# Performance work log

Hardware: AMD Instinct MI355X
Metric: run time of the kernel (lower is better)

The kernel has to match this reference:

```python
import jax, jax.numpy as jnp
import numpy as np

N_NODES = 100000
N_EDGES = 500000
H = 128
EPS = 1e-5


def _mlp(x, W1, b1, W2, b2, W3, b3, g, beta):
    # 3-layer MLP (ReLU) + final LayerNorm, matching build_mlp(..., lay_norm=True, n_layers=3)
    h = jax.nn.relu(x @ W1 + b1)
    h = jax.nn.relu(h @ W2 + b2)
    h = h @ W3 + b3
    mu = jnp.mean(h, axis=-1, keepdims=True)
    var = jnp.var(h, axis=-1, keepdims=True)
    return (h - mu) * jax.lax.rsqrt(var + EPS) * g + beta


def setup_inputs() -> dict:
    key = jax.random.key(0)
    ks = jax.random.split(key, 20)
    s = lambda fan_in: 1.0 / np.sqrt(fan_in)
    inp = {
        "x": jax.random.normal(ks[0], (N_NODES, H), dtype=jnp.float32),
        "edge_attr": jax.random.normal(ks[1], (N_EDGES, H), dtype=jnp.float32),
        "edge_index": jax.random.randint(ks[2], (2, N_EDGES), 0, N_NODES, dtype=jnp.int64),
        # Edge MLP: in = 3H
        "eW1": jax.random.normal(ks[3], (3 * H, H), dtype=jnp.float32) * s(3 * H),
        "eb1": jnp.zeros((H,), jnp.float32),
        "eW2": jax.random.normal(ks[4], (H, H), dtype=jnp.float32) * s(H),
        "eb2": jnp.zeros((H,), jnp.float32),
        "eW3": jax.random.normal(ks[5], (H, H), dtype=jnp.float32) * s(H),
        "eb3": jnp.zeros((H,), jnp.float32),
        "eg": jnp.ones((H,), jnp.float32),
        "ebeta": jnp.zeros((H,), jnp.float32),
        # Node MLP: in = 2H
        "nW1": jax.random.normal(ks[6], (2 * H, H), dtype=jnp.float32) * s(2 * H),
        "nb1": jnp.zeros((H,), jnp.float32),
        "nW2": jax.random.normal(ks[7], (H, H), dtype=jnp.float32) * s(H),
        "nb2": jnp.zeros((H,), jnp.float32),
        "nW3": jax.random.normal(ks[8], (H, H), dtype=jnp.float32) * s(H),
        "nb3": jnp.zeros((H,), jnp.float32),
        "ng": jnp.ones((H,), jnp.float32),
        "nbeta": jnp.zeros((H,), jnp.float32),
    }
    return inp


def reference(x, edge_attr, edge_index,
              eW1, eb1, eW2, eb2, eW3, eb3, eg, ebeta,
              nW1, nb1, nW2, nb2, nW3, nb3, ng, nbeta):
    senders = edge_index[0]
    receivers = edge_index[1]
    # EdgeBlock: gather src/dst node feats, concat with edge feats, MLP (3H -> H)
    e_in = jnp.concatenate([x[senders], x[receivers], edge_attr], axis=-1)
    e_new = _mlp(e_in, eW1, eb1, eW2, eb2, eW3, eb3, eg, ebeta)
    # NodeBlock: scatter-sum edge messages to receiver nodes, concat with node feats, MLP (2H -> H)
    agg = jax.ops.segment_sum(e_new, receivers, num_segments=N_NODES)
    n_in = jnp.concatenate([x, agg], axis=-1)
    x_new = _mlp(n_in, nW1, nb1, nW2, nb2, nW3, nb3, ng, nbeta)
    # Residual connections
    return (x + x_new, edge_attr + e_new)
```

## Files before the change

### kernel.cpp

```cpp
#include <hip/hip_runtime.h>

#define N_NODES 100000
#define N_EDGES 500000
#define H 128
#define EPS 1e-5f

typedef __attribute__((ext_vector_type(8))) short bf16x8;
typedef __attribute__((ext_vector_type(4))) float f32x4;

__device__ __forceinline__ unsigned short f2bf(float f) {
  unsigned int u = __builtin_bit_cast(unsigned int, f);
  u += 0x7FFFu + ((u >> 16) & 1u);
  return (unsigned short)(u >> 16);
}
__device__ __forceinline__ float bf2f(unsigned short u) {
  return __builtin_bit_cast(float, (unsigned)u << 16);
}

__device__ __forceinline__ int swz(int r, int k) {
  return r * 128 + (k ^ ((r & 7) << 3));
}

union PK8 { unsigned short u[8]; uint4 q; };

#define GLDS16(g, l)                                                        \
  __builtin_amdgcn_global_load_lds(                                         \
      (const __attribute__((address_space(1))) void*)(g),                   \
      (__attribute__((address_space(3))) void*)(l), 16, 0, 0)

__device__ __forceinline__ void stage_w512(unsigned short* dst,
                                           const unsigned short* img) {
  const int t = threadIdx.x;
  #pragma unroll
  for (int j = 0; j < 4; ++j)
    GLDS16((const char*)img + j * 8192 + t * 16, (char*)dst + j * 8192 + t * 16);
}

__device__ __forceinline__ void gemm_regA(const bf16x8 a[4], const unsigned short* Wb,
                                          int m0, int kq, f32x4 acc[8]) {
  #pragma unroll
  for (int kk = 0; kk < 4; ++kk) {
    const int k0 = kk * 32 + kq * 8;
    #pragma unroll
    for (int tc = 0; tc < 8; ++tc) {
      bf16x8 b = *(const bf16x8*)&Wb[swz(tc * 16 + m0, k0)];
      acc[tc] = __builtin_amdgcn_mfma_f32_16x16x32_bf16(a[kk], b, acc[tc], 0, 0, 0);
    }
  }
}

__device__ __forceinline__ void gemm_ldsA(const unsigned short* Hb, int wrow,
                                          const unsigned short* Wb,
                                          int m0, int kq, f32x4 acc[8]) {
  #pragma unroll
  for (int kk = 0; kk < 4; ++kk) {
    const int k0 = kk * 32 + kq * 8;
    bf16x8 a = *(const bf16x8*)&Hb[swz(wrow + m0, k0)];
    #pragma unroll
    for (int tc = 0; tc < 8; ++tc) {
      bf16x8 b = *(const bf16x8*)&Wb[swz(tc * 16 + m0, k0)];
      acc[tc] = __builtin_amdgcn_mfma_f32_16x16x32_bf16(a, b, acc[tc], 0, 0, 0);
    }
  }
}

__device__ __forceinline__ void zero_acc(f32x4 acc[8]) {
  #pragma unroll
  for (int b = 0; b < 8; ++b) acc[b] = (f32x4){0.f, 0.f, 0.f, 0.f};
}

__device__ __forceinline__ void write_h(unsigned short* Hb, const f32x4 acc[8],
                                        const float* __restrict__ bias,
                                        int wrow, int m0, int kq) {
  #pragma unroll
  for (int tc = 0; tc < 8; ++tc) {
    const int col = tc * 16 + m0;
    const float b = bias[col];
    #pragma unroll
    for (int i = 0; i < 4; ++i)
      Hb[swz(wrow + kq * 4 + i, col)] = f2bf(fmaxf(acc[tc][i] + b, 0.0f));
  }
}

__device__ __forceinline__ void ln4(const f32x4 acc[8], float mu[4], float rv[4]) {
  float s[4] = {0, 0, 0, 0}, ss[4] = {0, 0, 0, 0};
  #pragma unroll
  for (int tc = 0; tc < 8; ++tc)
    #pragma unroll
    for (int i = 0; i < 4; ++i) {
      const float v = acc[tc][i];
      s[i] += v;
      ss[i] += v * v;
    }
  #pragma unroll
  for (int off = 1; off < 16; off <<= 1)
    #pragma unroll
    for (int i = 0; i < 4; ++i) {
      s[i] += __shfl_xor(s[i], off);
      ss[i] += __shfl_xor(ss[i], off);
    }
  #pragma unroll
  for (int i = 0; i < 4; ++i) {
    const float m = s[i] * (1.0f / 128.0f);
    const float var = ss[i] * (1.0f / 128.0f) - m * m;
    mu[i] = m;
    rv[i] = rsqrtf(var + EPS);
  }
}


__global__ void xprep_kernel(const float* __restrict__ x,
                             unsigned short* __restrict__ xb) {
  const long i = (long)blockIdx.x * 256 + threadIdx.x;
  const long base = i * 8;
  if (base < (long)N_NODES * H) {
    float4 v0 = *(const float4*)(x + base);
    float4 v1 = *(const float4*)(x + base + 4);
    PK8 pk;
    pk.u[0] = f2bf(v0.x); pk.u[1] = f2bf(v0.y);
    pk.u[2] = f2bf(v0.z); pk.u[3] = f2bf(v0.w);
    pk.u[4] = f2bf(v1.x); pk.u[5] = f2bf(v1.y);
    pk.u[6] = f2bf(v1.z); pk.u[7] = f2bf(v1.w);
    *(uint4*)(xb + base) = pk.q;
  }
}

struct WSrc { const float* p[9]; };

__global__ void wprep_kernel(WSrc wsrc, unsigned short* __restrict__ wimg) {
  const int id = blockIdx.x * 256 + threadIdx.x;
  const int m = id >> 14;
  const int r = id & 16383;
  const int n = r & 127;
  const int k = r >> 7;
  wimg[m * 16384 + swz(n, k)] = f2bf(wsrc.p[m][k * 128 + n]);
}


__global__ void hist_kernel(const int* __restrict__ ridx, unsigned* __restrict__ cnt) {
  const int e = blockIdx.x * 256 + threadIdx.x;
  if (e < N_EDGES) atomicAdd(&cnt[ridx[e]], 1u);
}

__global__ void scan1_kernel(const unsigned* __restrict__ cnt,
                             unsigned* __restrict__ offs,
                             unsigned* __restrict__ part) {
  __shared__ unsigned sh[256];
  const int t = threadIdx.x;
  const int base = blockIdx.x * 1024 + t * 4;
  unsigned v[4];
  #pragma unroll
  for (int i = 0; i < 4; ++i) v[i] = (base + i < N_NODES) ? cnt[base + i] : 0u;
  unsigned pre[4];
  pre[0] = 0; pre[1] = v[0]; pre[2] = v[0] + v[1]; pre[3] = pre[2] + v[2];
  const unsigned tot = pre[3] + v[3];
  sh[t] = tot;
  __syncthreads();
  for (int d = 1; d < 256; d <<= 1) {
    const unsigned u_ = (t >= d) ? sh[t - d] : 0u;
    __syncthreads();
    sh[t] += u_;
    __syncthreads();
  }
  const unsigned excl = sh[t] - tot;
  #pragma unroll
  for (int i = 0; i < 4; ++i)
    if (base + i < N_NODES) offs[base + i] = excl + pre[i];
  if (t == 255) part[blockIdx.x] = sh[255];
}

__global__ void scan2_kernel(unsigned* __restrict__ part, int n) {
  __shared__ unsigned sh[128];
  const int t = threadIdx.x;
  const unsigned v = (t < n) ? part[t] : 0u;
  sh[t] = v;
  __syncthreads();
  for (int d = 1; d < 128; d <<= 1) {
    const unsigned u_ = (t >= d) ? sh[t - d] : 0u;
    __syncthreads();
    sh[t] += u_;
    __syncthreads();
  }
  if (t < n) part[t] = sh[t] - v;
}

__global__ void scan3_kernel(unsigned* __restrict__ offs,
                             const unsigned* __restrict__ part,
                             unsigned* __restrict__ cursor) {
  const int i = blockIdx.x * 256 + threadIdx.x;
  if (i < N_NODES) {
    const unsigned o = offs[i] + part[i >> 10];
    offs[i] = o;
    cursor[i] = o;
  }
  if (i == 0) offs[N_NODES] = N_EDGES;
}

__global__ void scatter_kernel(const int* __restrict__ ridx,
                               unsigned* __restrict__ cursor,
                               unsigned* __restrict__ eord) {
  const int e = blockIdx.x * 256 + threadIdx.x;
  if (e < N_EDGES) {
    const unsigned p = atomicAdd(&cursor[ridx[e]], 1u);
    eord[p] = (unsigned)e;
  }
}


__global__ __launch_bounds__(512, 4) void edge_kernel(
    const unsigned short* __restrict__ xb, const float* __restrict__ edge_attr,
    const int* __restrict__ eidx, const unsigned short* __restrict__ wimg,
    const float* __restrict__ eb1, const float* __restrict__ eb2,
    const float* __restrict__ eb3,
    const float* __restrict__ eg, const float* __restrict__ ebeta,
    float* __restrict__ out_e, unsigned short* __restrict__ enew) {
  __shared__ unsigned short Wbuf[128 * 128];
  __shared__ unsigned short Hbuf[128 * 128];

  const int t = threadIdx.x;
  const int lane = t & 63;
  const int wave = t >> 6;
  const int wrow = wave * 16;
  const int m0 = lane & 15;
  const int kq = lane >> 4;
  const long e0 = (long)blockIdx.x * 128;
  const int* sidx = eidx;
  const int* ridx = eidx + N_EDGES;

  stage_w512(Wbuf, wimg + 0L * 16384);
  stage_w512(Hbuf, wimg + 1L * 16384);

  long erow = e0 + wrow + m0;
  if (erow > N_EDGES - 1) erow = N_EDGES - 1;
  const long ns = sidx[erow];
  const long nr = ridx[erow];
  bf16x8 aS[4], aR[4];
  {
    const unsigned short* ps = xb + ns * H + kq * 8;
    const unsigned short* pr = xb + nr * H + kq * 8;
    #pragma unroll
    for (int kk = 0; kk < 4; ++kk) {
      aS[kk] = *(const bf16x8*)(ps + kk * 32);
      aR[kk] = *(const bf16x8*)(pr + kk * 32);
    }
  }

  f32x4 acc[8];
  zero_acc(acc);

  __syncthreads();
  gemm_regA(aS, Wbuf, m0, kq, acc);
  gemm_regA(aR, Hbuf, m0, kq, acc);

  bf16x8 aE[4];
  {
    const float* pe = edge_attr + erow * (long)H + kq * 8;
    #pragma unroll
    for (int kk = 0; kk < 4; ++kk) {
      float4 v0 = *(const float4*)(pe + kk * 32);
      float4 v1 = *(const float4*)(pe + kk * 32 + 4);
      PK8 pk;
      pk.u[0] = f2bf(v0.x); pk.u[1] = f2bf(v0.y);
      pk.u[2] = f2bf(v0.z); pk.u[3] = f2bf(v0.w);
      pk.u[4] = f2bf(v1.x); pk.u[5] = f2bf(v1.y);
      pk.u[6] = f2bf(v1.z); pk.u[7] = f2bf(v1.w);
      aE[kk] = __builtin_bit_cast(bf16x8, pk.q);
    }
  }

  __syncthreads();
  stage_w512(Wbuf, wimg + 2L * 16384);
  __syncthreads();
  gemm_regA(aE, Wbuf, m0, kq, acc);

  __syncthreads();
  stage_w512(Wbuf, wimg + 3L * 16384);
  write_h(Hbuf, acc, eb1, wrow, m0, kq);
  zero_acc(acc);
  __syncthreads();
  gemm_ldsA(Hbuf, wrow, Wbuf, m0, kq, acc);

  __syncthreads();
  stage_w512(Wbuf, wimg + 4L * 16384);
  write_h(Hbuf, acc, eb2, wrow, m0, kq);
  zero_acc(acc);
  __syncthreads();
  gemm_ldsA(Hbuf, wrow, Wbuf, m0, kq, acc);

  float gm[8], bt[8];
  #pragma unroll
  for (int tc = 0; tc < 8; ++tc) {
    const int col = tc * 16 + m0;
    const float b3 = eb3[col];
    gm[tc] = eg[col];
    bt[tc] = ebeta[col];
    #pragma unroll
    for (int i = 0; i < 4; ++i) acc[tc][i] += b3;
  }
  float mu[4], rv[4];
  ln4(acc, mu, rv);

  __syncthreads();
  #pragma unroll
  for (int tc = 0; tc < 8; ++tc) {
    const int col = tc * 16 + m0;
    #pragma unroll
    for (int i = 0; i < 4; ++i) {
      const float y = (acc[tc][i] - mu[i]) * rv[i] * gm[tc] + bt[tc];
      Hbuf[swz(wrow + kq * 4 + i, col)] = f2bf(y);
    }
  }
  __syncthreads();

  {
    const int r = t >> 2;
    const int c0 = (t & 3) * 32;
    const long e = e0 + r;
    if (e < N_EDGES) {
      const float* ea = edge_attr + e * (long)H + c0;
      float* oe = out_e + e * (long)H + c0;
      unsigned short* en = enew + e * (long)H + c0;
      #pragma unroll
      for (int c2 = 0; c2 < 4; ++c2) {
        uint4 qv = *(const uint4*)&Hbuf[swz(r, c0 + c2 * 8)];
        *(uint4*)(en + c2 * 8) = qv;
        const unsigned short* pu = (const unsigned short*)&qv;
        float4 a0 = *(const float4*)(ea + c2 * 8);
        float4 a1 = *(const float4*)(ea + c2 * 8 + 4);
        float4 o0, o1;
        o0.x = a0.x + bf2f(pu[0]); o0.y = a0.y + bf2f(pu[1]);
        o0.z = a0.z + bf2f(pu[2]); o0.w = a0.w + bf2f(pu[3]);
        o1.x = a1.x + bf2f(pu[4]); o1.y = a1.y + bf2f(pu[5]);
        o1.z = a1.z + bf2f(pu[6]); o1.w = a1.w + bf2f(pu[7]);
        *(float4*)(oe + c2 * 8) = o0;
        *(float4*)(oe + c2 * 8 + 4) = o1;
      }
    }
  }
}

__global__ __launch_bounds__(512, 4) void node_kernel(
    const unsigned short* __restrict__ xb, const float* __restrict__ x,
    const unsigned short* __restrict__ enew,
    const unsigned* __restrict__ offs, const unsigned* __restrict__ eord,
    const unsigned short* __restrict__ wimg,
    const float* __restrict__ nb1, const float* __restrict__ nb2,
    const float* __restrict__ nb3,
    const float* __restrict__ ng, const float* __restrict__ nbeta,
    float* __restrict__ out_x) {
  __shared__ unsigned short Wbuf[128 * 128];
  __shared__ unsigned short Hbuf[128 * 128];

  const int t = threadIdx.x;
  const int lane = t & 63;
  const int wave = t >> 6;
  const int wrow = wave * 16;
  const int m0 = lane & 15;
  const int kq = lane >> 4;
  const long n0 = (long)blockIdx.x * 128;

  stage_w512(Wbuf, wimg + 5L * 16384);

  long nrow = n0 + wrow + m0;
  if (nrow > N_NODES - 1) nrow = N_NODES - 1;
  bf16x8 aX[4];
  {
    const unsigned short* px = xb + nrow * H + kq * 8;
    #pragma unroll
    for (int kk = 0; kk < 4; ++kk) aX[kk] = *(const bf16x8*)(px + kk * 32);
  }

  float av[32];
  #pragma unroll
  for (int i = 0; i < 32; ++i) av[i] = 0.f;
  {
    const long sn = n0 + (t >> 2);
    if (sn < N_NODES) {
      const unsigned o0 = offs[sn], o1 = offs[sn + 1];
      const int c0 = (t & 3) * 32;
      for (unsigned u_ = o0; u_ < o1; ++u_) {
        const unsigned short* er = enew + (long)eord[u_] * H + c0;
        #pragma unroll
        for (int c2 = 0; c2 < 4; ++c2) {
          uint4 qv = *(const uint4*)(er + c2 * 8);
          const unsigned short* pu = (const unsigned short*)&qv;
          #pragma unroll
          for (int j = 0; j < 8; ++j) av[c2 * 8 + j] += bf2f(pu[j]);
        }
      }
    }
  }

  f32x4 acc[8];
  zero_acc(acc);

  __syncthreads();
  gemm_regA(aX, Wbuf, m0, kq, acc);
  __syncthreads();
  stage_w512(Wbuf, wimg + 6L * 16384);
  {
    const int r = t >> 2;
    const int c0 = (t & 3) * 32;
    #pragma unroll
    for (int c2 = 0; c2 < 4; ++c2) {
      PK8 pk;
      #pragma unroll
      for (int j = 0; j < 8; ++j) pk.u[j] = f2bf(av[c2 * 8 + j]);
      *(uint4*)&Hbuf[swz(r, c0 + c2 * 8)] = pk.q;
    }
  }
  __syncthreads();
  gemm_ldsA(Hbuf, wrow, Wbuf, m0, kq, acc);

  __syncthreads();
  stage_w512(Wbuf, wimg + 7L * 16384);
  write_h(Hbuf, acc, nb1, wrow, m0, kq);
  zero_acc(acc);
  __syncthreads();
  gemm_ldsA(Hbuf, wrow, Wbuf, m0, kq, acc);

  __syncthreads();
  stage_w512(Wbuf, wimg + 8L * 16384);
  write_h(Hbuf, acc, nb2, wrow, m0, kq);
  zero_acc(acc);
  __syncthreads();
  gemm_ldsA(Hbuf, wrow, Wbuf, m0, kq, acc);

  float gm[8], bt[8];
  #pragma unroll
  for (int tc = 0; tc < 8; ++tc) {
    const int col = tc * 16 + m0;
    const float b3 = nb3[col];
    gm[tc] = ng[col];
    bt[tc] = nbeta[col];
    #pragma unroll
    for (int i = 0; i < 4; ++i) acc[tc][i] += b3;
  }
  float mu[4], rv[4];
  ln4(acc, mu, rv);

  __syncthreads();
  #pragma unroll
  for (int tc = 0; tc < 8; ++tc) {
    const int col = tc * 16 + m0;
    #pragma unroll
    for (int i = 0; i < 4; ++i) {
      const float y = (acc[tc][i] - mu[i]) * rv[i] * gm[tc] + bt[tc];
      Hbuf[swz(wrow + kq * 4 + i, col)] = f2bf(y);
    }
  }
  __syncthreads();

  {
    const int r = t >> 2;
    const int c0 = (t & 3) * 32;
    const long n = n0 + r;
    if (n < N_NODES) {
      const float* xr = x + n * (long)H + c0;
      float* ox = out_x + n * (long)H + c0;
      #pragma unroll
      for (int c2 = 0; c2 < 4; ++c2) {
        uint4 qv = *(const uint4*)&Hbuf[swz(r, c0 + c2 * 8)];
        const unsigned short* pu = (const unsigned short*)&qv;
        float4 a0 = *(const float4*)(xr + c2 * 8);
        float4 a1 = *(const float4*)(xr + c2 * 8 + 4);
        float4 o0, o1;
        o0.x = a0.x + bf2f(pu[0]); o0.y = a0.y + bf2f(pu[1]);
        o0.z = a0.z + bf2f(pu[2]); o0.w = a0.w + bf2f(pu[3]);
        o1.x = a1.x + bf2f(pu[4]); o1.y = a1.y + bf2f(pu[5]);
        o1.z = a1.z + bf2f(pu[6]); o1.w = a1.w + bf2f(pu[7]);
        *(float4*)(ox + c2 * 8) = o0;
        *(float4*)(ox + c2 * 8 + 4) = o1;
      }
    }
  }
}

extern "C" void kernel_launch(void* const* d_in, const int* in_sizes, int n_in,
                              void* d_out, int out_size, void* d_ws, size_t ws_size,
                              hipStream_t stream) {
  (void)in_sizes; (void)n_in; (void)out_size; (void)ws_size;
  const float* x         = (const float*)d_in[0];
  const float* edge_attr = (const float*)d_in[1];
  const int*   eidx      = (const int*)d_in[2];
  const float* eW1 = (const float*)d_in[3];
  const float* eb1 = (const float*)d_in[4];
  const float* eW2 = (const float*)d_in[5];
  const float* eb2 = (const float*)d_in[6];
  const float* eW3 = (const float*)d_in[7];
  const float* eb3 = (const float*)d_in[8];
  const float* eg  = (const float*)d_in[9];
  const float* ebt = (const float*)d_in[10];
  const float* nW1 = (const float*)d_in[11];
  const float* nb1 = (const float*)d_in[12];
  const float* nW2 = (const float*)d_in[13];
  const float* nb2 = (const float*)d_in[14];
  const float* nW3 = (const float*)d_in[15];
  const float* nb3 = (const float*)d_in[16];
  const float* ng  = (const float*)d_in[17];
  const float* nbt = (const float*)d_in[18];

  float* out_x = (float*)d_out;
  float* out_e = (float*)d_out + (size_t)N_NODES * H;

  char* w = (char*)d_ws;
  unsigned short* enew = (unsigned short*)(w + 0);
  unsigned short* xb   = (unsigned short*)(w + 128000000);
  unsigned short* wimg = (unsigned short*)(w + 153600000);
  unsigned* offs   = (unsigned*)(w + 153894912);
  unsigned* cnt    = (unsigned*)(w + 154295040);
  unsigned* cursor = (unsigned*)(w + 154695168);
  unsigned* part   = (unsigned*)(w + 155095296);
  unsigned* eord   = (unsigned*)(w + 155096320);

  const int* ridx = eidx + N_EDGES;

  hipMemsetAsync(cnt, 0, (size_t)N_NODES * sizeof(unsigned), stream);

  WSrc wsrc;
  wsrc.p[0] = eW1;
  wsrc.p[1] = eW1 + 16384;
  wsrc.p[2] = eW1 + 32768;
  wsrc.p[3] = eW2;
  wsrc.p[4] = eW3;
  wsrc.p[5] = nW1;
  wsrc.p[6] = nW1 + 16384;
  wsrc.p[7] = nW2;
  wsrc.p[8] = nW3;

  xprep_kernel<<<(N_NODES * H / 8 + 255) / 256, 256, 0, stream>>>(x, xb);
  wprep_kernel<<<576, 256, 0, stream>>>(wsrc, wimg);

  hist_kernel<<<(N_EDGES + 255) / 256, 256, 0, stream>>>(ridx, cnt);
  scan1_kernel<<<(N_NODES + 1023) / 1024, 256, 0, stream>>>(cnt, offs, part);
  scan2_kernel<<<1, 128, 0, stream>>>(part, (N_NODES + 1023) / 1024);
  scan3_kernel<<<(N_NODES + 255) / 256, 256, 0, stream>>>(offs, part, cursor);
  scatter_kernel<<<(N_EDGES + 255) / 256, 256, 0, stream>>>(ridx, cursor, eord);

  const int eblocks = (N_EDGES + 127) / 128;
  const int nblocks = (N_NODES + 127) / 128;
  edge_kernel<<<eblocks, 512, 0, stream>>>(xb, edge_attr, eidx, wimg, eb1, eb2, eb3,
                                           eg, ebt, out_e, enew);
  node_kernel<<<nblocks, 512, 0, stream>>>(xb, x, enew, offs, eord, wimg,
                                           nb1, nb2, nb3, ng, nbt, out_x);
}
```

Before: 459.0 us.

## Precompute per-node first-layer projections and use persistent CSR-sorted edge/node kernels

```diff
diff --git a/kernel.cpp b/kernel.cpp
--- a/kernel.cpp
+++ b/kernel.cpp
@@ -4,6 +4,9 @@
 #define N_EDGES 500000
 #define H 128
 #define EPS 1e-5f
+#define NT_E 1954
+#define NT_N 391
+#define PGRID 256
 
 typedef __attribute__((ext_vector_type(8))) short bf16x8;
 typedef __attribute__((ext_vector_type(4))) float f32x4;
@@ -28,14 +31,6 @@
       (const __attribute__((address_space(1))) void*)(g),                   \
       (__attribute__((address_space(3))) void*)(l), 16, 0, 0)
 
-__device__ __forceinline__ void stage_w512(unsigned short* dst,
-                                           const unsigned short* img) {
-  const int t = threadIdx.x;
-  #pragma unroll
-  for (int j = 0; j < 4; ++j)
-    GLDS16((const char*)img + j * 8192 + t * 16, (char*)dst + j * 8192 + t * 16);
-}
-
 __device__ __forceinline__ void gemm_regA(const bf16x8 a[4], const unsigned short* Wb,
                                           int m0, int kq, f32x4 acc[8]) {
   #pragma unroll
@@ -67,19 +62,6 @@
 __device__ __forceinline__ void zero_acc(f32x4 acc[8]) {
   #pragma unroll
   for (int b = 0; b < 8; ++b) acc[b] = (f32x4){0.f, 0.f, 0.f, 0.f};
-}
-
-__device__ __forceinline__ void write_h(unsigned short* Hb, const f32x4 acc[8],
-                                        const float* __restrict__ bias,
-                                        int wrow, int m0, int kq) {
-  #pragma unroll
-  for (int tc = 0; tc < 8; ++tc) {
-    const int col = tc * 16 + m0;
-    const float b = bias[col];
-    #pragma unroll
-    for (int i = 0; i < 4; ++i)
-      Hb[swz(wrow + kq * 4 + i, col)] = f2bf(fmaxf(acc[tc][i] + b, 0.0f));
-  }
 }
 
 __device__ __forceinline__ void ln4(const f32x4 acc[8], float mu[4], float rv[4]) {
@@ -108,22 +90,6 @@
   }
 }
 
-
-__global__ void xprep_kernel(const float* __restrict__ x,
-                             unsigned short* __restrict__ xb) {
-  const long i = (long)blockIdx.x * 256 + threadIdx.x;
-  const long base = i * 8;
-  if (base < (long)N_NODES * H) {
-    float4 v0 = *(const float4*)(x + base);
-    float4 v1 = *(const float4*)(x + base + 4);
-    PK8 pk;
-    pk.u[0] = f2bf(v0.x); pk.u[1] = f2bf(v0.y);
-    pk.u[2] = f2bf(v0.z); pk.u[3] = f2bf(v0.w);
-    pk.u[4] = f2bf(v1.x); pk.u[5] = f2bf(v1.y);
-    pk.u[6] = f2bf(v1.z); pk.u[7] = f2bf(v1.w);
-    *(uint4*)(xb + base) = pk.q;
-  }
-}
 
 struct WSrc { const float* p[9]; };
 
@@ -134,6 +100,86 @@
   const int n = r & 127;
   const int k = r >> 7;
   wimg[m * 16384 + swz(n, k)] = f2bf(wsrc.p[m][k * 128 + n]);
+}
+
+
+__global__ __launch_bounds__(512, 2) void px_kernel(
+    const float* __restrict__ x, const unsigned short* __restrict__ wimg,
+    const float* __restrict__ eb1, const float* __restrict__ nb1,
+    unsigned short* __restrict__ pxs, unsigned short* __restrict__ pxr,
+    unsigned short* __restrict__ pxn) {
+  extern __shared__ unsigned short smem[];
+  const int t = threadIdx.x;
+  #pragma unroll
+  for (int j = 0; j < 12; ++j)
+    GLDS16((const char*)wimg + j * 8192 + t * 16, (char*)smem + j * 8192 + t * 16);
+  __syncthreads();
+
+  const int lane = t & 63;
+  const int wtile = (t >> 6) * 16;
+  const int m0 = lane & 15;
+  const int kq = lane >> 4;
+  const long n0 = (long)blockIdx.x * 128;
+
+  long an = n0 + wtile + m0;
+  if (an > N_NODES - 1) an = N_NODES - 1;
+  const float* px_ = x + an * H + kq * 8;
+  bf16x8 aX[4];
+  #pragma unroll
+  for (int kk = 0; kk < 4; ++kk) {
+    float4 v0 = *(const float4*)(px_ + kk * 32);
+    float4 v1 = *(const float4*)(px_ + kk * 32 + 4);
+    PK8 pk;
+    pk.u[0] = f2bf(v0.x); pk.u[1] = f2bf(v0.y);
+    pk.u[2] = f2bf(v0.z); pk.u[3] = f2bf(v0.w);
+    pk.u[4] = f2bf(v1.x); pk.u[5] = f2bf(v1.y);
+    pk.u[6] = f2bf(v1.z); pk.u[7] = f2bf(v1.w);
+    aX[kk] = __builtin_bit_cast(bf16x8, pk.q);
+  }
+  const long cb = n0 + wtile + kq * 4;
+
+  f32x4 acc[8];
+  float bv[8];
+  zero_acc(acc);
+  gemm_regA(aX, smem, m0, kq, acc);
+  #pragma unroll
+  for (int tc = 0; tc < 8; ++tc) bv[tc] = eb1[tc * 16 + m0];
+  #pragma unroll
+  for (int i = 0; i < 4; ++i) {
+    const long nn = cb + i;
+    if (nn < N_NODES) {
+      PK8 pk;
+      #pragma unroll
+      for (int tc = 0; tc < 8; ++tc) pk.u[tc] = f2bf(acc[tc][i] + bv[tc]);
+      *(uint4*)(pxs + nn * H + m0 * 8) = pk.q;
+    }
+  }
+  zero_acc(acc);
+  gemm_regA(aX, smem + 16384, m0, kq, acc);
+  #pragma unroll
+  for (int i = 0; i < 4; ++i) {
+    const long nn = cb + i;
+    if (nn < N_NODES) {
+      PK8 pk;
+      #pragma unroll
+      for (int tc = 0; tc < 8; ++tc) pk.u[tc] = f2bf(acc[tc][i]);
+      *(uint4*)(pxr + nn * H + m0 * 8) = pk.q;
+    }
+  }
+  zero_acc(acc);
+  gemm_regA(aX, smem + 32768, m0, kq, acc);
+  #pragma unroll
+  for (int tc = 0; tc < 8; ++tc) bv[tc] = nb1[tc * 16 + m0];
+  #pragma unroll
+  for (int i = 0; i < 4; ++i) {
+    const long nn = cb + i;
+    if (nn < N_NODES) {
+      PK8 pk;
+      #pragma unroll
+      for (int tc = 0; tc < 8; ++tc) pk.u[tc] = f2bf(acc[tc][i] + bv[tc]);
+      *(uint4*)(pxn + nn * H + m0 * 8) = pk.q;
+    }
+  }
 }
 
 
@@ -198,63 +244,53 @@
 
 __global__ void scatter_kernel(const int* __restrict__ ridx,
                                unsigned* __restrict__ cursor,
-                               unsigned* __restrict__ eord) {
+                               int* __restrict__ slot) {
   const int e = blockIdx.x * 256 + threadIdx.x;
-  if (e < N_EDGES) {
-    const unsigned p = atomicAdd(&cursor[ridx[e]], 1u);
-    eord[p] = (unsigned)e;
-  }
-}
-
-
-__global__ __launch_bounds__(512, 4) void edge_kernel(
-    const unsigned short* __restrict__ xb, const float* __restrict__ edge_attr,
-    const int* __restrict__ eidx, const unsigned short* __restrict__ wimg,
-    const float* __restrict__ eb1, const float* __restrict__ eb2,
-    const float* __restrict__ eb3,
+  if (e < N_EDGES) slot[e] = (int)atomicAdd(&cursor[ridx[e]], 1u);
+}
+
+
+__global__ __launch_bounds__(1024, 4) void edge_kernel(
+    const float* __restrict__ edge_attr, const int* __restrict__ eidx,
+    const int* __restrict__ slot, const unsigned short* __restrict__ wimg,
+    const unsigned short* __restrict__ pxs, const unsigned short* __restrict__ pxr,
+    const float* __restrict__ eb2, const float* __restrict__ eb3,
     const float* __restrict__ eg, const float* __restrict__ ebeta,
     float* __restrict__ out_e, unsigned short* __restrict__ enew) {
-  __shared__ unsigned short Wbuf[128 * 128];
-  __shared__ unsigned short Hbuf[128 * 128];
-
+  extern __shared__ unsigned short smem[];
+  unsigned short* Wc = smem;
+  unsigned short* W2 = smem + 16384;
+  unsigned short* W3 = smem + 32768;
+  unsigned short* Hb = smem + 49152;
   const int t = threadIdx.x;
+  #pragma unroll
+  for (int j = 0; j < 6; ++j)
+    GLDS16((const char*)(wimg + 3 * 16384) + j * 16384 + t * 16,
+           (char*)smem + j * 16384 + t * 16);
+  __syncthreads();
+
   const int lane = t & 63;
-  const int wave = t >> 6;
-  const int wrow = wave * 16;
+  const int wtile = (t >> 6) * 16;
   const int m0 = lane & 15;
   const int kq = lane >> 4;
-  const long e0 = (long)blockIdx.x * 128;
   const int* sidx = eidx;
   const int* ridx = eidx + N_EDGES;
 
-  stage_w512(Wbuf, wimg + 0L * 16384);
-  stage_w512(Hbuf, wimg + 1L * 16384);
-
-  long erow = e0 + wrow + m0;
-  if (erow > N_EDGES - 1) erow = N_EDGES - 1;
-  const long ns = sidx[erow];
-  const long nr = ridx[erow];
-  bf16x8 aS[4], aR[4];
-  {
-    const unsigned short* ps = xb + ns * H + kq * 8;
-    const unsigned short* pr = xb + nr * H + kq * 8;
-    #pragma unroll
-    for (int kk = 0; kk < 4; ++kk) {
-      aS[kk] = *(const bf16x8*)(ps + kk * 32);
-      aR[kk] = *(const bf16x8*)(pr + kk * 32);
-    }
-  }
-
-  f32x4 acc[8];
-  zero_acc(acc);
-
-  __syncthreads();
-  gemm_regA(aS, Wbuf, m0, kq, acc);
-  gemm_regA(aR, Hbuf, m0, kq, acc);
-
-  bf16x8 aE[4];
-  {
-    const float* pe = edge_attr + erow * (long)H + kq * 8;
+  for (int tile = blockIdx.x; tile < NT_E; tile += PGRID) {
+    const long e0 = (long)tile * 256;
+    const long cb = e0 + wtile + kq * 4;
+    const long cbl = cb > (long)(N_EDGES - 4) ? (long)(N_EDGES - 4) : cb;
+    int4 s4 = *(const int4*)&sidx[cbl];
+    int4 r4 = *(const int4*)&ridx[cbl];
+    int4 p4 = *(const int4*)&slot[cbl];
+    const int* sp = (const int*)&s4;
+    const int* rp = (const int*)&r4;
+    const int* pp = (const int*)&p4;
+
+    long ae = e0 + wtile + m0;
+    if (ae > N_EDGES - 1) ae = N_EDGES - 1;
+    const float* pe = edge_attr + ae * H + kq * 8;
+    bf16x8 aE[4];
     #pragma unroll
     for (int kk = 0; kk < 4; ++kk) {
       float4 v0 = *(const float4*)(pe + kk * 32);
@@ -266,211 +302,195 @@
       pk.u[6] = f2bf(v1.z); pk.u[7] = f2bf(v1.w);
       aE[kk] = __builtin_bit_cast(bf16x8, pk.q);
     }
-  }
-
-  __syncthreads();
-  stage_w512(Wbuf, wimg + 2L * 16384);
-  __syncthreads();
-  gemm_regA(aE, Wbuf, m0, kq, acc);
-
-  __syncthreads();
-  stage_w512(Wbuf, wimg + 3L * 16384);
-  write_h(Hbuf, acc, eb1, wrow, m0, kq);
-  zero_acc(acc);
-  __syncthreads();
-  gemm_ldsA(Hbuf, wrow, Wbuf, m0, kq, acc);
-
-  __syncthreads();
-  stage_w512(Wbuf, wimg + 4L * 16384);
-  write_h(Hbuf, acc, eb2, wrow, m0, kq);
-  zero_acc(acc);
-  __syncthreads();
-  gemm_ldsA(Hbuf, wrow, Wbuf, m0, kq, acc);
-
-  float gm[8], bt[8];
-  #pragma unroll
-  for (int tc = 0; tc < 8; ++tc) {
-    const int col = tc * 16 + m0;
-    const float b3 = eb3[col];
-    gm[tc] = eg[col];
-    bt[tc] = ebeta[col];
-    #pragma unroll
-    for (int i = 0; i < 4; ++i) acc[tc][i] += b3;
-  }
-  float mu[4], rv[4];
-  ln4(acc, mu, rv);
-
-  __syncthreads();
-  #pragma unroll
-  for (int tc = 0; tc < 8; ++tc) {
-    const int col = tc * 16 + m0;
-    #pragma unroll
-    for (int i = 0; i < 4; ++i) {
-      const float y = (acc[tc][i] - mu[i]) * rv[i] * gm[tc] + bt[tc];
-      Hbuf[swz(wrow + kq * 4 + i, col)] = f2bf(y);
-    }
-  }
-  __syncthreads();
-
-  {
-    const int r = t >> 2;
-    const int c0 = (t & 3) * 32;
-    const long e = e0 + r;
-    if (e < N_EDGES) {
-      const float* ea = edge_attr + e * (long)H + c0;
-      float* oe = out_e + e * (long)H + c0;
-      unsigned short* en = enew + e * (long)H + c0;
-      #pragma unroll
-      for (int c2 = 0; c2 < 4; ++c2) {
-        uint4 qv = *(const uint4*)&Hbuf[swz(r, c0 + c2 * 8)];
-        *(uint4*)(en + c2 * 8) = qv;
-        const unsigned short* pu = (const unsigned short*)&qv;
-        float4 a0 = *(const float4*)(ea + c2 * 8);
-        float4 a1 = *(const float4*)(ea + c2 * 8 + 4);
-        float4 o0, o1;
-        o0.x = a0.x + bf2f(pu[0]); o0.y = a0.y + bf2f(pu[1]);
-        o0.z = a0.z + bf2f(pu[2]); o0.w = a0.w + bf2f(pu[3]);
-        o1.x = a1.x + bf2f(pu[4]); o1.y = a1.y + bf2f(pu[5]);
-        o1.z = a1.z + bf2f(pu[6]); o1.w = a1.w + bf2f(pu[7]);
-        *(float4*)(oe + c2 * 8) = o0;
-        *(float4*)(oe + c2 * 8 + 4) = o1;
+    uint4 qs[4], qr[4];
+    #pragma unroll
+    for (int i = 0; i < 4; ++i) {
+      qs[i] = *(const uint4*)(pxs + (long)sp[i] * H + m0 * 8);
+      qr[i] = *(const uint4*)(pxr + (long)rp[i] * H + m0 * 8);
+    }
+
+    f32x4 acc[8];
+    zero_acc(acc);
+    gemm_regA(aE, Wc, m0, kq, acc);
+    #pragma unroll
+    for (int i = 0; i < 4; ++i) {
+      const unsigned short* us = (const unsigned short*)&qs[i];
+      const unsigned short* ur = (const unsigned short*)&qr[i];
+      #pragma unroll
+      for (int tc = 0; tc < 8; ++tc)
+        acc[tc][i] += bf2f(us[tc]) + bf2f(ur[tc]);
+    }
+    #pragma unroll
+    for (int tc = 0; tc < 8; ++tc) {
+      const int col = tc * 16 + m0;
+      #pragma unroll
+      for (int i = 0; i < 4; ++i)
+        Hb[swz(wtile + kq * 4 + i, col)] = f2bf(fmaxf(acc[tc][i], 0.f));
+    }
+    zero_acc(acc);
+    gemm_ldsA(Hb, wtile, W2, m0, kq, acc);
+    float b2v[8];
+    #pragma unroll
+    for (int tc = 0; tc < 8; ++tc) b2v[tc] = eb2[tc * 16 + m0];
+    #pragma unroll
+    for (int tc = 0; tc < 8; ++tc) {
+      const int col = tc * 16 + m0;
+      #pragma unroll
+      for (int i = 0; i < 4; ++i)
+        Hb[swz(wtile + kq * 4 + i, col)] = f2bf(fmaxf(acc[tc][i] + b2v[tc], 0.f));
+    }
+    zero_acc(acc);
+    gemm_ldsA(Hb, wtile, W3, m0, kq, acc);
+
+    float b3v[8], gv[8], btv[8];
+    #pragma unroll
+    for (int tc = 0; tc < 8; ++tc) {
+      const int col = tc * 16 + m0;
+      b3v[tc] = eb3[col];
+      gv[tc] = eg[col];
+      btv[tc] = ebeta[col];
+    }
+    #pragma unroll
+    for (int tc = 0; tc < 8; ++tc)
+      #pragma unroll
+      for (int i = 0; i < 4; ++i) acc[tc][i] += b3v[tc];
+    float mu[4], rv[4];
+    ln4(acc, mu, rv);
+
+    #pragma unroll
+    for (int i = 0; i < 4; ++i) {
+      const long er = cb + i;
+      if (er < N_EDGES) {
+        const long ps = (long)pp[i] * H;
+        #pragma unroll
+        for (int tc = 0; tc < 8; ++tc) {
+          const int col = tc * 16 + m0;
+          const float y = (acc[tc][i] - mu[i]) * rv[i] * gv[tc] + btv[tc];
+          out_e[er * H + col] = edge_attr[er * H + col] + y;
+          enew[ps + col] = f2bf(y);
+        }
       }
     }
   }
 }
 
-__global__ __launch_bounds__(512, 4) void node_kernel(
-    const unsigned short* __restrict__ xb, const float* __restrict__ x,
-    const unsigned short* __restrict__ enew,
-    const unsigned* __restrict__ offs, const unsigned* __restrict__ eord,
-    const unsigned short* __restrict__ wimg,
-    const float* __restrict__ nb1, const float* __restrict__ nb2,
-    const float* __restrict__ nb3,
+__global__ __launch_bounds__(1024, 4) void node_kernel(
+    const float* __restrict__ x, const unsigned short* __restrict__ enew,
+    const unsigned* __restrict__ offs, const unsigned short* __restrict__ wimg,
+    const unsigned short* __restrict__ pxn,
+    const float* __restrict__ nb2, const float* __restrict__ nb3,
     const float* __restrict__ ng, const float* __restrict__ nbeta,
     float* __restrict__ out_x) {
-  __shared__ unsigned short Wbuf[128 * 128];
-  __shared__ unsigned short Hbuf[128 * 128];
-
+  extern __shared__ unsigned short smem[];
+  unsigned short* W1 = smem;
+  unsigned short* W2 = smem + 16384;
+  unsigned short* W3 = smem + 32768;
+  unsigned short* Hb = smem + 49152;
   const int t = threadIdx.x;
+  #pragma unroll
+  for (int j = 0; j < 6; ++j)
+    GLDS16((const char*)(wimg + 6 * 16384) + j * 16384 + t * 16,
+           (char*)smem + j * 16384 + t * 16);
+  __syncthreads();
+
   const int lane = t & 63;
-  const int wave = t >> 6;
-  const int wrow = wave * 16;
+  const int wtile = (t >> 6) * 16;
   const int m0 = lane & 15;
   const int kq = lane >> 4;
-  const long n0 = (long)blockIdx.x * 128;
-
-  stage_w512(Wbuf, wimg + 5L * 16384);
-
-  long nrow = n0 + wrow + m0;
-  if (nrow > N_NODES - 1) nrow = N_NODES - 1;
-  bf16x8 aX[4];
-  {
-    const unsigned short* px = xb + nrow * H + kq * 8;
-    #pragma unroll
-    for (int kk = 0; kk < 4; ++kk) aX[kk] = *(const bf16x8*)(px + kk * 32);
-  }
-
-  float av[32];
-  #pragma unroll
-  for (int i = 0; i < 32; ++i) av[i] = 0.f;
-  {
-    const long sn = n0 + (t >> 2);
-    if (sn < N_NODES) {
-      const unsigned o0 = offs[sn], o1 = offs[sn + 1];
-      const int c0 = (t & 3) * 32;
-      for (unsigned u_ = o0; u_ < o1; ++u_) {
-        const unsigned short* er = enew + (long)eord[u_] * H + c0;
+
+  for (int tile = blockIdx.x; tile < NT_N; tile += PGRID) {
+    const long n0 = (long)tile * 256;
+    long an = n0 + wtile + m0;
+    if (an > N_NODES - 1) an = N_NODES - 1;
+    const unsigned o0 = offs[an], o1 = offs[an + 1];
+
+    float sm[4][8];
+    #pragma unroll
+    for (int kk = 0; kk < 4; ++kk)
+      #pragma unroll
+      for (int c = 0; c < 8; ++c) sm[kk][c] = 0.f;
+    for (unsigned j = o0; j < o1; ++j) {
+      const unsigned short* er = enew + (long)j * H + kq * 8;
+      #pragma unroll
+      for (int kk = 0; kk < 4; ++kk) {
+        uint4 q = *(const uint4*)(er + kk * 32);
+        const unsigned short* pu = (const unsigned short*)&q;
         #pragma unroll
-        for (int c2 = 0; c2 < 4; ++c2) {
-          uint4 qv = *(const uint4*)(er + c2 * 8);
-          const unsigned short* pu = (const unsigned short*)&qv;
-          #pragma unroll
-          for (int j = 0; j < 8; ++j) av[c2 * 8 + j] += bf2f(pu[j]);
+        for (int c = 0; c < 8; ++c) sm[kk][c] += bf2f(pu[c]);
+      }
+    }
+    bf16x8 aG[4];
+    #pragma unroll
+    for (int kk = 0; kk < 4; ++kk) {
+      PK8 pk;
+      #pragma unroll
+      for (int c = 0; c < 8; ++c) pk.u[c] = f2bf(sm[kk][c]);
+      aG[kk] = __builtin_bit_cast(bf16x8, pk.q);
+    }
+
+    const long cb = n0 + wtile + kq * 4;
+    const long cbl = cb > (long)(N_NODES - 4) ? (long)(N_NODES - 4) : cb;
+    uint4 qn[4];
+    #pragma unroll
+    for (int i = 0; i < 4; ++i)
+      qn[i] = *(const uint4*)(pxn + (cbl + i) * H + m0 * 8);
+
+    f32x4 acc[8];
+    zero_acc(acc);
+    gemm_regA(aG, W1, m0, kq, acc);
+    #pragma unroll
+    for (int i = 0; i < 4; ++i) {
+      const unsigned short* un = (const unsigned short*)&qn[i];
+      #pragma unroll
+      for (int tc = 0; tc < 8; ++tc) acc[tc][i] += bf2f(un[tc]);
+    }
+    #pragma unroll
+    for (int tc = 0; tc < 8; ++tc) {
+      const int col = tc * 16 + m0;
+      #pragma unroll
+      for (int i = 0; i < 4; ++i)
+        Hb[swz(wtile + kq * 4 + i, col)] = f2bf(fmaxf(acc[tc][i], 0.f));
+    }
+    zero_acc(acc);
+    gemm_ldsA(Hb, wtile, W2, m0, kq, acc);
+    float b2v[8];
+    #pragma unroll
+    for (int tc = 0; tc < 8; ++tc) b2v[tc] = nb2[tc * 16 + m0];
+    #pragma unroll
+    for (int tc = 0; tc < 8; ++tc) {
+      const int col = tc * 16 + m0;
+      #pragma unroll
+      for (int i = 0; i < 4; ++i)
+        Hb[swz(wtile + kq * 4 + i, col)] = f2bf(fmaxf(acc[tc][i] + b2v[tc], 0.f));
+    }
+    zero_acc(acc);
+    gemm_ldsA(Hb, wtile, W3, m0, kq, acc);
+
+    float b3v[8], gv[8], btv[8];
+    #pragma unroll
+    for (int tc = 0; tc < 8; ++tc) {
+      const int col = tc * 16 + m0;
+      b3v[tc] = nb3[col];
+      gv[tc] = ng[col];
+      btv[tc] = nbeta[col];
+    }
+    #pragma unroll
+    for (int tc = 0; tc < 8; ++tc)
+      #pragma unroll
+      for (int i = 0; i < 4; ++i) acc[tc][i] += b3v[tc];
+    float mu[4], rv[4];
+    ln4(acc, mu, rv);
+
+    #pragma unroll
+    for (int i = 0; i < 4; ++i) {
+      const long nn = cb + i;
+      if (nn < N_NODES) {
+        #pragma unroll
+        for (int tc = 0; tc < 8; ++tc) {
+          const int col = tc * 16 + m0;
+          const float y = (acc[tc][i] - mu[i]) * rv[i] * gv[tc] + btv[tc];
+          out_x[nn * H + col] = x[nn * H + col] + y;
         }
-      }
-    }
-  }
-
-  f32x4 acc[8];
-  zero_acc(acc);
-
-  __syncthreads();
-  gemm_regA(aX, Wbuf, m0, kq, acc);
-  __syncthreads();
-  stage_w512(Wbuf, wimg + 6L * 16384);
-  {
-    const int r = t >> 2;
-    const int c0 = (t & 3) * 32;
-    #pragma unroll
-    for (int c2 = 0; c2 < 4; ++c2) {
-      PK8 pk;
-      #pragma unroll
-      for (int j = 0; j < 8; ++j) pk.u[j] = f2bf(av[c2 * 8 + j]);
-      *(uint4*)&Hbuf[swz(r, c0 + c2 * 8)] = pk.q;
-    }
-  }
-  __syncthreads();
-  gemm_ldsA(Hbuf, wrow, Wbuf, m0, kq, acc);
-
-  __syncthreads();
-  stage_w512(Wbuf, wimg + 7L * 16384);
-  write_h(Hbuf, acc, nb1, wrow, m0, kq);
-  zero_acc(acc);
-  __syncthreads();
-  gemm_ldsA(Hbuf, wrow, Wbuf, m0, kq, acc);
-
-  __syncthreads();
-  stage_w512(Wbuf, wimg + 8L * 16384);
-  write_h(Hbuf, acc, nb2, wrow, m0, kq);
-  zero_acc(acc);
-  __syncthreads();
-  gemm_ldsA(Hbuf, wrow, Wbuf, m0, kq, acc);
-
-  float gm[8], bt[8];
-  #pragma unroll
-  for (int tc = 0; tc < 8; ++tc) {
-    const int col = tc * 16 + m0;
-    const float b3 = nb3[col];
-    gm[tc] = ng[col];
-    bt[tc] = nbeta[col];
-    #pragma unroll
-    for (int i = 0; i < 4; ++i) acc[tc][i] += b3;
-  }
-  float mu[4], rv[4];
-  ln4(acc, mu, rv);
-
-  __syncthreads();
-  #pragma unroll
-  for (int tc = 0; tc < 8; ++tc) {
-    const int col = tc * 16 + m0;
-    #pragma unroll
-    for (int i = 0; i < 4; ++i) {
-      const float y = (acc[tc][i] - mu[i]) * rv[i] * gm[tc] + bt[tc];
-      Hbuf[swz(wrow + kq * 4 + i, col)] = f2bf(y);
-    }
-  }
-  __syncthreads();
-
-  {
-    const int r = t >> 2;
-    const int c0 = (t & 3) * 32;
-    const long n = n0 + r;
-    if (n < N_NODES) {
-      const float* xr = x + n * (long)H + c0;
-      float* ox = out_x + n * (long)H + c0;
-      #pragma unroll
-      for (int c2 = 0; c2 < 4; ++c2) {
-        uint4 qv = *(const uint4*)&Hbuf[swz(r, c0 + c2 * 8)];
-        const unsigned short* pu = (const unsigned short*)&qv;
-        float4 a0 = *(const float4*)(xr + c2 * 8);
-        float4 a1 = *(const float4*)(xr + c2 * 8 + 4);
-        float4 o0, o1;
-        o0.x = a0.x + bf2f(pu[0]); o0.y = a0.y + bf2f(pu[1]);
-        o0.z = a0.z + bf2f(pu[2]); o0.w = a0.w + bf2f(pu[3]);
-        o1.x = a1.x + bf2f(pu[4]); o1.y = a1.y + bf2f(pu[5]);
-        o1.z = a1.z + bf2f(pu[6]); o1.w = a1.w + bf2f(pu[7]);
-        *(float4*)(ox + c2 * 8) = o0;
-        *(float4*)(ox + c2 * 8 + 4) = o1;
       }
     }
   }
@@ -505,42 +525,51 @@
 
   char* w = (char*)d_ws;
   unsigned short* enew = (unsigned short*)(w + 0);
-  unsigned short* xb   = (unsigned short*)(w + 128000000);
-  unsigned short* wimg = (unsigned short*)(w + 153600000);
-  unsigned* offs   = (unsigned*)(w + 153894912);
-  unsigned* cnt    = (unsigned*)(w + 154295040);
-  unsigned* cursor = (unsigned*)(w + 154695168);
-  unsigned* part   = (unsigned*)(w + 155095296);
-  unsigned* eord   = (unsigned*)(w + 155096320);
+  unsigned short* pxs  = (unsigned short*)(w + 128000000);
+  unsigned short* pxr  = (unsigned short*)(w + 153600000);
+  unsigned short* pxn  = (unsigned short*)(w + 179200000);
+  unsigned short* wimg = (unsigned short*)(w + 204800000);
+  unsigned* offs   = (unsigned*)(w + 205094912);
+  unsigned* cnt    = (unsigned*)(w + 205495040);
+  unsigned* cursor = (unsigned*)(w + 205895168);
+  unsigned* part   = (unsigned*)(w + 206295296);
+  int* slot        = (int*)(w + 206296320);
 
   const int* ridx = eidx + N_EDGES;
+
+  hipFuncSetAttribute((const void*)px_kernel,
+                      hipFuncAttributeMaxDynamicSharedMemorySize, 98304);
+  hipFuncSetAttribute((const void*)edge_kernel,
+                      hipFuncAttributeMaxDynamicSharedMemorySize, 163840);
+  hipFuncSetAttribute((const void*)node_kernel,
+                      hipFuncAttributeMaxDynamicSharedMemorySize, 163840);
 
   hipMemsetAsync(cnt, 0, (size_t)N_NODES * sizeof(unsigned), stream);
 
   WSrc wsrc;
   wsrc.p[0] = eW1;
   wsrc.p[1] = eW1 + 16384;
-  wsrc.p[2] = eW1 + 32768;
-  wsrc.p[3] = eW2;
-  wsrc.p[4] = eW3;
-  wsrc.p[5] = nW1;
+  wsrc.p[2] = nW1;
+  wsrc.p[3] = eW1 + 32768;
+  wsrc.p[4] = eW2;
+  wsrc.p[5] = eW3;
   wsrc.p[6] = nW1 + 16384;
   wsrc.p[7] = nW2;
   wsrc.p[8] = nW3;
-
-  xprep_kernel<<<(N_NODES * H / 8 + 255) / 256, 256, 0, stream>>>(x, xb);
   wprep_kernel<<<576, 256, 0, stream>>>(wsrc, wimg);
+
+  px_kernel<<<(N_NODES + 127) / 128, 512, 98304, stream>>>(x, wimg, eb1, nb1,
+                                                           pxs, pxr, pxn);
 
   hist_kernel<<<(N_EDGES + 255) / 256, 256, 0, stream>>>(ridx, cnt);
   scan1_kernel<<<(N_NODES + 1023) / 1024, 256, 0, stream>>>(cnt, offs, part);
   scan2_kernel<<<1, 128, 0, stream>>>(part, (N_NODES + 1023) / 1024);
   scan3_kernel<<<(N_NODES + 255) / 256, 256, 0, stream>>>(offs, part, cursor);
-  scatter_kernel<<<(N_EDGES + 255) / 256, 256, 0, stream>>>(ridx, cursor, eord);
-
-  const int eblocks = (N_EDGES + 127) / 128;
-  const int nblocks = (N_NODES + 127) / 128;
-  edge_kernel<<<eblocks, 512, 0, stream>>>(xb, edge_attr, eidx, wimg, eb1, eb2, eb3,
-                                           eg, ebt, out_e, enew);
-  node_kernel<<<nblocks, 512, 0, stream>>>(xb, x, enew, offs, eord, wimg,
-                                           nb1, nb2, nb3, ng, nbt, out_x);
-}
+  scatter_kernel<<<(N_EDGES + 255) / 256, 256, 0, stream>>>(ridx, cursor, slot);
+
+  edge_kernel<<<PGRID, 1024, 163840, stream>>>(edge_attr, eidx, slot, wimg,
+                                               pxs, pxr, eb2, eb3, eg, ebt,
+                                               out_e, enew);
+  node_kernel<<<PGRID, 1024, 163840, stream>>>(x, enew, offs, wimg, pxn,
+                                               nb2, nb3, ng, nbt, out_x);
+}
```

After: 495.7 us. 8.0% more time.
